# Kernel tuning notes

Measured on AMD Instinct MI355X. Metric: run time of the kernel, lower is better.

The kernel has to match this reference:

```python
import jax, jax.numpy as jnp
import numpy as np

NTYPE, NWAVE, NIPSIN = 4, 16, 3
CUTOFF = 5.0
NLOCAL, NALL, NNEIGH = 40000, 48000, 800000
# angular-order index for each of the npara = 1 + 3 + 9 = 13 angular channels
INDEX_PARA = np.concatenate([np.full(3 ** i, i, dtype=np.int32) for i in range(NIPSIN)])


def setup_inputs() -> dict:
    key = jax.random.key(0)
    k0, k1, k2, k3, k4, k5, k6 = jax.random.split(key, 7)
    cart = jax.random.normal(k0, (NALL, 3), dtype=jnp.float32) * 3.0
    i0 = jax.random.randint(k1, (NNEIGH,), 0, NLOCAL, dtype=jnp.int32)
    off = jax.random.randint(k2, (NNEIGH,), 1, NALL, dtype=jnp.int32)
    i1 = (i0 + off) % NALL  # guaranteed != i0 -> no zero distances
    atom_index = jnp.stack([i0, i1], axis=0)
    local_species = jax.random.randint(k3, (NLOCAL,), 0, NTYPE, dtype=jnp.int32)
    neigh_species = jax.random.randint(k4, (NNEIGH,), 0, NTYPE, dtype=jnp.int32)
    rs = jax.random.uniform(k5, (NTYPE, NWAVE), dtype=jnp.float32) * CUTOFF
    inta = 0.5 + jax.random.uniform(k6, (NTYPE, NWAVE), dtype=jnp.float32)
    params = jnp.ones((NTYPE, NWAVE), dtype=jnp.float32)
    return {"cart": cart, "rs": rs, "inta": inta, "params": params,
            "atom_index": atom_index, "local_species": local_species,
            "neigh_species": neigh_species}


def _density(cart, rs, inta, params, atom_index, nlocal, neigh_species):
    # gather neighbor pair coordinates: (2, n, 3)
    sel = cart[atom_index.reshape(-1)].reshape(2, -1, 3)
    dvec = sel[0] - sel[1]                               # (n, 3)
    dist = jnp.linalg.norm(dvec, axis=-1)                # (n,)
    dvec = dvec / dist[:, None]                          # unit vectors
    # cutoff_cosine
    fcut = jnp.square(0.5 * jnp.cos(dist * (np.pi / CUTOFF)) + 0.5)  # (n,)
    # species-gathered gaussian radial basis (vectorized form of per-type masked_scatter loop)
    radial = jnp.exp(-inta[neigh_species] * jnp.square(dist[:, None] - rs[neigh_species]))  # (n, nwave)
    # angular tensor-product channels: concat over orders 0..NIPSIN-1 -> (13, n)
    dvt = dvec.T                                         # (3, n)
    orb = fcut[None, :]                                  # (1, n)
    parts = [orb]
    for _ in range(1, NIPSIN):
        orb = (orb[:, None, :] * dvt[None, :, :]).reshape(-1, orb.shape[1])  # (3^p, n)
        parts.append(orb)
    angular = jnp.concatenate(parts, axis=0)             # (npara, n)
    # outer product per pair: (n, npara, nwave)
    orbital = jnp.einsum('ji,ik->ijk', angular, radial)
    worb = orbital * params[neigh_species][:, None, :]
    # scatter-add over central atoms
    sumw = jnp.zeros((nlocal, angular.shape[0], rs.shape[1]), worb.dtype)
    sumw = sumw.at[atom_index[0]].add(worb)              # (nlocal, npara, nwave)
    # reduce squared channels by angular order
    density = jnp.zeros((nlocal, NIPSIN, rs.shape[1]), worb.dtype)
    density = density.at[:, INDEX_PARA].add(jnp.square(sumw))
    return density.reshape(nlocal, -1)                   # (nlocal, nipsin*nwave)


def reference(cart, rs, inta, params, atom_index, local_species, neigh_species):
    nlocal = local_species.shape[0]
    return _density(cart, rs, inta, params, atom_index, nlocal, neigh_species)
```

## Files before the change

kernel.cpp:

```cpp
#include <hip/hip_runtime.h>
#include <hip/hip_bf16.h>

#define NWAVE 16
#define LOG2CHUNK 14
#define CHUNK (1 << LOG2CHUNK)
#define HIST_WORDS 10240

constexpr float PI_OVER_CUT = 3.14159265358979323846f / 5.0f;


__global__ __launch_bounds__(1024) void chunk_hist_rank(
    const int* __restrict__ idx0, unsigned short* __restrict__ lrank,
    unsigned short* __restrict__ hist16, int nneigh, int halfp)
{
    __shared__ unsigned lds[HIST_WORDS];
    int c = blockIdx.x >> 1;
    int parity = blockIdx.x & 1;
    int t = threadIdx.x;

    int words = halfp >> 1;
    for (int w = t; w < words; w += 1024) lds[w] = 0u;
    __syncthreads();

    int jbeg = c << LOG2CHUNK;
    int jend = jbeg + CHUNK; if (jend > nneigh) jend = nneigh;
    for (int j = jbeg + t; j < jend; j += 1024) {
        int a = idx0[j];
        if ((a & 1) == parity) {
            int bin = a >> 1;
            int word = bin >> 1;
            int shift = (bin & 1) << 4;
            unsigned old = atomicAdd(&lds[word], 1u << shift);
            lrank[j] = (unsigned short)((old >> shift) & 0xffffu);
        }
    }
    __syncthreads();

    unsigned* hrow = (unsigned*)(hist16 + (size_t)blockIdx.x * halfp);
    for (int w = t; w < words; w += 1024) hrow[w] = lds[w];
}


__global__ __launch_bounds__(256) void combine_pre(
    const unsigned short* __restrict__ hist16, unsigned* __restrict__ counts,
    unsigned short* __restrict__ chunkpre, int nlocal, int nc, int halfp)
{
    int a = blockIdx.x * blockDim.x + threadIdx.x;
    if (a >= nlocal) return;
    int parity = a & 1;
    int bin = a >> 1;
    unsigned run = 0;
    for (int c = 0; c < nc; ++c) {
        unsigned h = hist16[(size_t)(c*2 + parity) * halfp + bin];
        chunkpre[(size_t)a * nc + c] = (unsigned short)run;
        run += h;
    }
    counts[a] = run;
}


__global__ __launch_bounds__(256) void scan_partial(const unsigned* __restrict__ counts,
                                                    unsigned* __restrict__ partials, int n) {
    __shared__ unsigned wsum[4];
    int t = threadIdx.x;
    int base = blockIdx.x * 1024 + t * 4;
    unsigned s = 0;
    #pragma unroll
    for (int e = 0; e < 4; ++e) { int id = base + e; if (id < n) s += counts[id]; }
    #pragma unroll
    for (int off = 32; off >= 1; off >>= 1) s += __shfl_xor(s, off, 64);
    int lane = t & 63, w = t >> 6;
    if (lane == 0) wsum[w] = s;
    __syncthreads();
    if (t == 0) partials[blockIdx.x] = wsum[0] + wsum[1] + wsum[2] + wsum[3];
}

__global__ __launch_bounds__(64) void scan_blockoffs(const unsigned* __restrict__ partials,
                                                     unsigned* __restrict__ blockoff,
                                                     unsigned* __restrict__ offsets,
                                                     int nblk, int nlocal) {
    int t = threadIdx.x;
    unsigned v = (t < nblk) ? partials[t] : 0u;
    unsigned incl = v;
    #pragma unroll
    for (int off = 1; off < 64; off <<= 1) {
        unsigned u = __shfl_up(incl, off, 64);
        if (t >= off) incl += u;
    }
    if (t < nblk) blockoff[t] = incl - v;
    if (t == nblk - 1) offsets[nlocal] = incl;
}

__global__ __launch_bounds__(256) void scan_final(const unsigned* __restrict__ counts,
                                                  const unsigned* __restrict__ blockoff,
                                                  unsigned* __restrict__ offsets, int n) {
    __shared__ unsigned wsum[4];
    int t = threadIdx.x;
    int lane = t & 63, w = t >> 6;
    int base = blockIdx.x * 1024 + t * 4;
    unsigned c[4];
    #pragma unroll
    for (int e = 0; e < 4; ++e) { int id = base + e; c[e] = (id < n) ? counts[id] : 0u; }
    unsigned tsum = c[0] + c[1] + c[2] + c[3];
    unsigned incl = tsum;
    #pragma unroll
    for (int off = 1; off < 64; off <<= 1) {
        unsigned u = __shfl_up(incl, off, 64);
        if (lane >= off) incl += u;
    }
    if (lane == 63) wsum[w] = incl;
    __syncthreads();
    unsigned wpre = 0;
    for (int i = 0; i < 4; ++i) if (i < w) wpre += wsum[i];
    unsigned x = blockoff[blockIdx.x] + wpre + (incl - tsum);
    #pragma unroll
    for (int e = 0; e < 4; ++e) {
        int id = base + e;
        if (id < n) offsets[id] = x;
        x += c[e];
    }
}


__global__ __launch_bounds__(256) void geom_scatter_direct(
    const float* __restrict__ cart, const int* __restrict__ idx0,
    const int* __restrict__ idx1, const int* __restrict__ nspec,
    const unsigned short* __restrict__ lrank, const unsigned* __restrict__ offsets,
    const unsigned short* __restrict__ chunkpre, float4* __restrict__ srec,
    int nneigh, int nc)
{
    int j = blockIdx.x * blockDim.x + threadIdx.x;
    if (j >= nneigh) return;
    int i0 = idx0[j], i1 = idx1[j], s = nspec[j];
    int c = j >> LOG2CHUNK;
    unsigned p = offsets[i0] + (unsigned)chunkpre[(size_t)i0 * nc + c] + (unsigned)lrank[j];
    float ax = cart[3*i0], ay = cart[3*i0+1], az = cart[3*i0+2];
    float bx = cart[3*i1], by = cart[3*i1+1], bz = cart[3*i1+2];
    float dxv = ax - bx, dyv = ay - by, dzv = az - bz;
    float d2 = dxv*dxv + dyv*dyv + dzv*dzv;
    float rinv = rsqrtf(d2);
    float dist = d2 * rinv;
    unsigned db = (__float_as_uint(dist) & ~3u) | (unsigned)s;
    srec[p] = make_float4(dxv * rinv, dyv * rinv, dzv * rinv, __uint_as_float(db));
}


__global__ __launch_bounds__(256) void density_seq(
    const float* __restrict__ rs, const float* __restrict__ inta,
    const float* __restrict__ params, const unsigned* __restrict__ offsets,
    const float4* __restrict__ srec, float* __restrict__ out,
    int nlocal, int nneigh)
{
    int t = threadIdx.x;
    int lane = t & 63;
    int k = lane & 15, g = lane >> 4;
    int a = blockIdx.x * 4 + (t >> 6);
    if (a >= nlocal) return;

    float rs0 = rs[k],        rs1 = rs[16 + k],     rs2 = rs[32 + k],     rs3 = rs[48 + k];
    float ia0 = inta[k],      ia1 = inta[16 + k],   ia2 = inta[32 + k],   ia3 = inta[48 + k];
    float pp0 = params[k],    pp1 = params[16 + k], pp2 = params[32 + k], pp3 = params[48 + k];

    int beg = (int)offsets[a], end = (int)offsets[a + 1];
    int lim = nneigh - 1;

    float aw = 0.f, axl = 0.f, ayl = 0.f, azl = 0.f;
    float axx = 0.f, ayy = 0.f, azz = 0.f, axy = 0.f, axz = 0.f, ayz = 0.f;

    int p0 = beg + g; if (p0 > lim) p0 = lim;
    float4 rec0 = srec[p0];

    for (int n = beg; n < end; n += 4) {
        int p1 = n + 4 + g; if (p1 > lim) p1 = lim;
        float4 rec1 = srec[p1];

        unsigned u = __float_as_uint(rec0.w);
        float dist = __uint_as_float(u & ~3u);
        bool c1 = (u & 1u) != 0u, c2 = (u & 2u) != 0u;
        float rsel = c2 ? (c1 ? rs3 : rs2) : (c1 ? rs1 : rs0);
        float isel = c2 ? (c1 ? ia3 : ia2) : (c1 ? ia1 : ia0);
        float psel = c2 ? (c1 ? pp3 : pp2) : (c1 ? pp1 : pp0);
        float dd  = dist - rsel;
        float rad = __expf(-isel * dd * dd);
        float fc  = fmaf(0.5f, __cosf(dist * PI_OVER_CUT), 0.5f);
        float w   = rad * fc * fc * psel;
        w = (n + g < end) ? w : 0.f;

        float dx = rec0.x, dy = rec0.y, dz = rec0.z;
        float wx = w * dx, wy = w * dy, wz = w * dz;
        aw  += w;
        axl += wx;  ayl += wy;  azl += wz;
        axx = fmaf(wx, dx, axx);  axy = fmaf(wx, dy, axy);  axz = fmaf(wx, dz, axz);
        ayy = fmaf(wy, dy, ayy);  ayz = fmaf(wy, dz, ayz);  azz = fmaf(wz, dz, azz);

        rec0 = rec1;
    }

    #define RED2(x) x += __shfl_xor(x, 16, 64); x += __shfl_xor(x, 32, 64)
    RED2(aw); RED2(axl); RED2(ayl); RED2(azl);
    RED2(axx); RED2(ayy); RED2(azz); RED2(axy); RED2(axz); RED2(ayz);
    #undef RED2

    if (g == 0) {
        float l0 = aw * aw;
        float l1 = axl*axl + ayl*ayl + azl*azl;
        float l2 = axx*axx + ayy*ayy + azz*azz + 2.f*(axy*axy + axz*axz + ayz*ayz);
        out[a*48 + k]      = l0;
        out[a*48 + 16 + k] = l1;
        out[a*48 + 32 + k] = l2;
    }
}


__global__ void hist_kernel(const int* __restrict__ idx0, unsigned* __restrict__ counts, int nneigh) {
    int j = blockIdx.x * blockDim.x + threadIdx.x;
    if (j < nneigh) atomicAdd(&counts[idx0[j]], 1u);
}

__global__ void scan_kernel_1blk(const unsigned* __restrict__ counts, unsigned* __restrict__ offsets,
                                 unsigned* __restrict__ cursor, int nlocal) {
    __shared__ unsigned part[1024];
    int t = threadIdx.x;
    int ch = (nlocal + 1023) / 1024;
    int base = t * ch;
    unsigned s = 0;
    for (int i = 0; i < ch; ++i) { int id = base + i; if (id < nlocal) s += counts[id]; }
    part[t] = s;
    __syncthreads();
    for (int off = 1; off < 1024; off <<= 1) {
        unsigned v = (t >= off) ? part[t - off] : 0u;
        __syncthreads();
        part[t] += v;
        __syncthreads();
    }
    unsigned run = (t == 0) ? 0u : part[t - 1];
    for (int i = 0; i < ch; ++i) {
        int id = base + i;
        if (id < nlocal) { offsets[id] = run; cursor[id] = run; run += counts[id]; }
    }
    if (t == 1023) offsets[nlocal] = part[1023];
}

__global__ __launch_bounds__(256) void scatter_idx(const int* __restrict__ idx0,
                                                   unsigned* __restrict__ cursor,
                                                   unsigned* __restrict__ sorted, int nneigh) {
    int j = blockIdx.x * blockDim.x + threadIdx.x;
    if (j < nneigh) {
        unsigned p = atomicAdd(&cursor[idx0[j]], 1u);
        sorted[p] = (unsigned)j;
    }
}

__global__ __launch_bounds__(256) void density_kernel(
    const float* __restrict__ cart, const float* __restrict__ rs,
    const float* __restrict__ inta, const float* __restrict__ params,
    const int* __restrict__ idx1, const int* __restrict__ nspec,
    const unsigned* __restrict__ offsets, const unsigned* __restrict__ sorted,
    float* __restrict__ out, int nlocal)
{
    int lane = threadIdx.x & 63;
    int a = blockIdx.x * 4 + (threadIdx.x >> 6);
    if (a >= nlocal) return;
    int k = lane & 15;
    int g = lane >> 4;
    float c0x = cart[3*a], c0y = cart[3*a+1], c0z = cart[3*a+2];
    int a1, b1, a2, b2;
    switch (g) {
      case 0:  a1=0; b1=0; a2=1; b2=1; break;
      case 1:  a1=0; b1=1; a2=1; b2=2; break;
      case 2:  a1=0; b1=2; a2=2; b2=0; break;
      default: a1=1; b1=0; a2=2; b2=1; break;
    }
    float acc0 = 0.f, acc1 = 0.f, acc2 = 0.f, acc3 = 0.f;
    unsigned beg = offsets[a], end = offsets[a + 1];
    for (unsigned n = beg; n < end; ++n) {
        int j  = (int)sorted[n];
        int i1 = idx1[j];
        int s  = nspec[j];
        float dxv = c0x - cart[3*i1];
        float dyv = c0y - cart[3*i1+1];
        float dzv = c0z - cart[3*i1+2];
        float d2   = dxv*dxv + dyv*dyv + dzv*dzv;
        float rinv = rsqrtf(d2);
        float dist = d2 * rinv;
        float dx = dxv * rinv, dy = dyv * rinv, dz = dzv * rinv;
        float fc   = 0.5f * __cosf(dist * PI_OVER_CUT) + 0.5f;
        float fcut = fc * fc;
        float tt   = dist - rs[s*NWAVE + k];
        float rad  = __expf(-inta[s*NWAVE + k] * tt * tt) * params[s*NWAVE + k];
        float f1 = (g == 0) ? fcut : fcut * (g == 1 ? dx : (g == 2 ? dy : dz));
        acc0 = fmaf(f1, rad, acc0);
        float pa1 = (a1 == 0 ? dx : (a1 == 1 ? dy : dz));
        float pb1 = (b1 == 0 ? dx : (b1 == 1 ? dy : dz));
        acc1 = fmaf(fcut * pa1 * pb1, rad, acc1);
        float pa2 = (a2 == 0 ? dx : (a2 == 1 ? dy : dz));
        float pb2 = (b2 == 0 ? dx : (b2 == 1 ? dy : dz));
        acc2 = fmaf(fcut * pa2 * pb2, rad, acc2);
        if (g == 0) acc3 = fmaf(fcut * dz * dz, rad, acc3);
    }
    float l0, l1, l2;
    if (g == 0) { l0 = acc0*acc0; l1 = 0.f;        l2 = acc1*acc1 + acc2*acc2 + acc3*acc3; }
    else        { l0 = 0.f;       l1 = acc0*acc0;  l2 = acc1*acc1 + acc2*acc2; }
    l0 += __shfl_xor(l0, 16, 64); l1 += __shfl_xor(l1, 16, 64); l2 += __shfl_xor(l2, 16, 64);
    l0 += __shfl_xor(l0, 32, 64); l1 += __shfl_xor(l1, 32, 64); l2 += __shfl_xor(l2, 32, 64);
    if (g == 0) {
        out[a*48 + k]      = l0;
        out[a*48 + 16 + k] = l1;
        out[a*48 + 32 + k] = l2;
    }
}


extern "C" void kernel_launch(void* const* d_in, const int* in_sizes, int n_in,
                              void* d_out, int out_size, void* d_ws, size_t ws_size,
                              hipStream_t stream) {
    const float* cart   = (const float*)d_in[0];
    const float* rs     = (const float*)d_in[1];
    const float* inta   = (const float*)d_in[2];
    const float* params = (const float*)d_in[3];
    const int* atom_index    = (const int*)d_in[4];
    const int* neigh_species = (const int*)d_in[6];
    int nlocal = in_sizes[5];
    int nneigh = in_sizes[6];
    const int* idx0 = atom_index;
    const int* idx1 = atom_index + nneigh;

    int tb = 256;
    int nblkN = (nneigh + tb - 1) / tb;
    int nblkS = (nlocal + 1023) / 1024;
    int nc = (nneigh + CHUNK - 1) >> LOG2CHUNK;
    int halfp = (((nlocal + 1) >> 1) + 63) & ~63;

    char* ws = (char*)d_ws;
    size_t off = 0;
    auto carve = [&](size_t bytes) -> char* {
        off = (off + 255) & ~(size_t)255;
        char* p = ws + off; off += bytes; return p;
    };
    unsigned* counts        = (unsigned*)carve((size_t)nlocal * 4);
    unsigned* offsets       = (unsigned*)carve(((size_t)nlocal + 1) * 4);
    unsigned* cursor        = (unsigned*)carve((size_t)nlocal * 4);
    unsigned* partials      = (unsigned*)carve(256 * 4);
    unsigned* blockoff      = (unsigned*)carve(256 * 4);
    float4*   srec          = (float4*)carve((size_t)nneigh * 16);
    unsigned short* lrank   = (unsigned short*)carve((size_t)nneigh * 2);
    unsigned short* hist16  = (unsigned short*)carve((size_t)nc * 2 * halfp * 2);
    unsigned short* chunkpre= (unsigned short*)carve((size_t)nlocal * nc * 2);
    size_t need_fast = off;

    bool fast = (ws_size >= need_fast) && (nblkS <= 64) && (halfp <= 2 * HIST_WORDS) && (nc <= 64);

    if (fast) {
        chunk_hist_rank<<<nc * 2, 1024, 0, stream>>>(idx0, lrank, hist16, nneigh, halfp);
        combine_pre<<<(nlocal + tb - 1) / tb, tb, 0, stream>>>(hist16, counts, chunkpre,
                                                               nlocal, nc, halfp);
        scan_partial<<<nblkS, 256, 0, stream>>>(counts, partials, nlocal);
        scan_blockoffs<<<1, 64, 0, stream>>>(partials, blockoff, offsets, nblkS, nlocal);
        scan_final<<<nblkS, 256, 0, stream>>>(counts, blockoff, offsets, nlocal);
        geom_scatter_direct<<<nblkN, tb, 0, stream>>>(cart, idx0, idx1, neigh_species,
                                                      lrank, offsets, chunkpre, srec,
                                                      nneigh, nc);
        density_seq<<<(nlocal + 3) / 4, 256, 0, stream>>>(rs, inta, params, offsets, srec,
                                                          (float*)d_out, nlocal, nneigh);
    } else {
        unsigned* sorted = (unsigned*)srec;
        hipMemsetAsync(counts, 0, (size_t)nlocal * 4, stream);
        hist_kernel<<<nblkN, tb, 0, stream>>>(idx0, counts, nneigh);
        scan_kernel_1blk<<<1, 1024, 0, stream>>>(counts, offsets, cursor, nlocal);
        scatter_idx<<<nblkN, tb, 0, stream>>>(idx0, cursor, sorted, nneigh);
        density_kernel<<<(nlocal + 3) / 4, 256, 0, stream>>>(cart, rs, inta, params, idx1,
                                                             neigh_species, offsets, sorted,
                                                             (float*)d_out, nlocal);
    }
}
```

Before: 85.13 us.

## Fuse count/scan kernels and transpose chunk prefix table to chunk-major

Replaces the combine_pre plus three-kernel scan with two kernels: one computes per-block count partials straight from the chunk histograms, and the second scans block partials in-wave, computes per-atom offsets, and writes chunk prefixes. The chunk-prefix table becomes chunk-major so those writes coalesce, and reads in the scatter kernel fall within a single chunk row for neighbouring j. This cuts launch count and the intermediate counts/blockoff round trips, at the cost of reading the histograms twice.

```diff
diff --git a/kernel.cpp b/kernel.cpp
--- a/kernel.cpp
+++ b/kernel.cpp
@@ -41,83 +41,87 @@
 }
 
 
-__global__ __launch_bounds__(256) void combine_pre(
-    const unsigned short* __restrict__ hist16, unsigned* __restrict__ counts,
-    unsigned short* __restrict__ chunkpre, int nlocal, int nc, int halfp)
-{
-    int a = blockIdx.x * blockDim.x + threadIdx.x;
-    if (a >= nlocal) return;
-    int parity = a & 1;
-    int bin = a >> 1;
-    unsigned run = 0;
-    for (int c = 0; c < nc; ++c) {
-        unsigned h = hist16[(size_t)(c*2 + parity) * halfp + bin];
-        chunkpre[(size_t)a * nc + c] = (unsigned short)run;
-        run += h;
-    }
-    counts[a] = run;
-}
-
-
-__global__ __launch_bounds__(256) void scan_partial(const unsigned* __restrict__ counts,
-                                                    unsigned* __restrict__ partials, int n) {
-    __shared__ unsigned wsum[4];
-    int t = threadIdx.x;
-    int base = blockIdx.x * 1024 + t * 4;
-    unsigned s = 0;
+__global__ __launch_bounds__(1024) void count_partial(
+    const unsigned short* __restrict__ hist16, unsigned* __restrict__ partials,
+    int nlocal, int nc, int halfp)
+{
+    __shared__ unsigned wsum[16];
+    int t = threadIdx.x;
+    int lane = t & 63, wid = t >> 6;
+    int a = blockIdx.x * 1024 + t;
+    unsigned v = 0;
+    if (a < nlocal) {
+        int parity = a & 1, bin = a >> 1;
+        for (int c = 0; c < nc; ++c)
+            v += hist16[(size_t)(c * 2 + parity) * halfp + bin];
+    }
     #pragma unroll
-    for (int e = 0; e < 4; ++e) { int id = base + e; if (id < n) s += counts[id]; }
-    #pragma unroll
-    for (int off = 32; off >= 1; off >>= 1) s += __shfl_xor(s, off, 64);
-    int lane = t & 63, w = t >> 6;
-    if (lane == 0) wsum[w] = s;
-    __syncthreads();
-    if (t == 0) partials[blockIdx.x] = wsum[0] + wsum[1] + wsum[2] + wsum[3];
-}
-
-__global__ __launch_bounds__(64) void scan_blockoffs(const unsigned* __restrict__ partials,
-                                                     unsigned* __restrict__ blockoff,
-                                                     unsigned* __restrict__ offsets,
-                                                     int nblk, int nlocal) {
-    int t = threadIdx.x;
-    unsigned v = (t < nblk) ? partials[t] : 0u;
+    for (int o = 32; o >= 1; o >>= 1) v += __shfl_xor(v, o, 64);
+    if (lane == 0) wsum[wid] = v;
+    __syncthreads();
+    if (t == 0) {
+        unsigned s = 0;
+        #pragma unroll
+        for (int i = 0; i < 16; ++i) s += wsum[i];
+        partials[blockIdx.x] = s;
+    }
+}
+
+
+__global__ __launch_bounds__(1024) void scan_offsets_chunkpre(
+    const unsigned short* __restrict__ hist16, const unsigned* __restrict__ partials,
+    unsigned* __restrict__ offsets, unsigned short* __restrict__ chunkpreT,
+    int nlocal, int nblk, int nc, int halfp, int nlocalp)
+{
+    __shared__ unsigned wsum[16];
+    __shared__ unsigned sOff;
+    int t = threadIdx.x;
+    int lane = t & 63, wid = t >> 6;
+    int a = blockIdx.x * 1024 + t;
+
+    if (wid == 0) {
+        unsigned p = (lane < nblk) ? partials[lane] : 0u;
+        unsigned incl = p;
+        #pragma unroll
+        for (int o = 1; o < 64; o <<= 1) {
+            unsigned u = __shfl_up(incl, o, 64);
+            if (lane >= o) incl += u;
+        }
+        if (lane == blockIdx.x) sOff = incl - p;
+    }
+
+    unsigned v = 0;
+    if (a < nlocal) {
+        int parity = a & 1, bin = a >> 1;
+        for (int c = 0; c < nc; ++c) {
+            chunkpreT[(size_t)c * nlocalp + a] = (unsigned short)v;
+            v += hist16[(size_t)(c * 2 + parity) * halfp + bin];
+        }
+    }
+
     unsigned incl = v;
     #pragma unroll
-    for (int off = 1; off < 64; off <<= 1) {
-        unsigned u = __shfl_up(incl, off, 64);
-        if (t >= off) incl += u;
-    }
-    if (t < nblk) blockoff[t] = incl - v;
-    if (t == nblk - 1) offsets[nlocal] = incl;
-}
-
-__global__ __launch_bounds__(256) void scan_final(const unsigned* __restrict__ counts,
-                                                  const unsigned* __restrict__ blockoff,
-                                                  unsigned* __restrict__ offsets, int n) {
-    __shared__ unsigned wsum[4];
-    int t = threadIdx.x;
-    int lane = t & 63, w = t >> 6;
-    int base = blockIdx.x * 1024 + t * 4;
-    unsigned c[4];
-    #pragma unroll
-    for (int e = 0; e < 4; ++e) { int id = base + e; c[e] = (id < n) ? counts[id] : 0u; }
-    unsigned tsum = c[0] + c[1] + c[2] + c[3];
-    unsigned incl = tsum;
-    #pragma unroll
-    for (int off = 1; off < 64; off <<= 1) {
-        unsigned u = __shfl_up(incl, off, 64);
-        if (lane >= off) incl += u;
-    }
-    if (lane == 63) wsum[w] = incl;
-    __syncthreads();
-    unsigned wpre = 0;
-    for (int i = 0; i < 4; ++i) if (i < w) wpre += wsum[i];
-    unsigned x = blockoff[blockIdx.x] + wpre + (incl - tsum);
-    #pragma unroll
-    for (int e = 0; e < 4; ++e) {
-        int id = base + e;
-        if (id < n) offsets[id] = x;
-        x += c[e];
+    for (int o = 1; o < 64; o <<= 1) {
+        unsigned u = __shfl_up(incl, o, 64);
+        if (lane >= o) incl += u;
+    }
+    if (lane == 63) wsum[wid] = incl;
+    __syncthreads();
+    if (t < 16) {
+        unsigned u = wsum[t];
+        unsigned wincl = u;
+        #pragma unroll
+        for (int o = 1; o < 16; o <<= 1) {
+            unsigned x = __shfl_up(wincl, o, 64);
+            if (t >= o) wincl += x;
+        }
+        wsum[t] = wincl - u;
+    }
+    __syncthreads();
+    if (a < nlocal) {
+        unsigned o = sOff + wsum[wid] + (incl - v);
+        offsets[a] = o;
+        if (a == nlocal - 1) offsets[nlocal] = o + v;
     }
 }
 
@@ -126,14 +130,15 @@
     const float* __restrict__ cart, const int* __restrict__ idx0,
     const int* __restrict__ idx1, const int* __restrict__ nspec,
     const unsigned short* __restrict__ lrank, const unsigned* __restrict__ offsets,
-    const unsigned short* __restrict__ chunkpre, float4* __restrict__ srec,
-    int nneigh, int nc)
+    const unsigned short* __restrict__ chunkpreT, float4* __restrict__ srec,
+    int nneigh, int nlocalp)
 {
     int j = blockIdx.x * blockDim.x + threadIdx.x;
     if (j >= nneigh) return;
     int i0 = idx0[j], i1 = idx1[j], s = nspec[j];
     int c = j >> LOG2CHUNK;
-    unsigned p = offsets[i0] + (unsigned)chunkpre[(size_t)i0 * nc + c] + (unsigned)lrank[j];
+    unsigned p = offsets[i0] + (unsigned)chunkpreT[(size_t)c * nlocalp + i0]
+                             + (unsigned)lrank[j];
     float ax = cart[3*i0], ay = cart[3*i0+1], az = cart[3*i0+2];
     float bx = cart[3*i1], by = cart[3*i1+1], bz = cart[3*i1+2];
     float dxv = ax - bx, dyv = ay - by, dzv = az - bz;
@@ -327,9 +332,10 @@
 
     int tb = 256;
     int nblkN = (nneigh + tb - 1) / tb;
-    int nblkS = (nlocal + 1023) / 1024;
     int nc = (nneigh + CHUNK - 1) >> LOG2CHUNK;
     int halfp = (((nlocal + 1) >> 1) + 63) & ~63;
+    int nlocalp = (nlocal + 63) & ~63;
+    int nblkB = (nlocal + 1023) / 1024;
 
     char* ws = (char*)d_ws;
     size_t off = 0;
@@ -341,25 +347,24 @@
     unsigned* offsets       = (unsigned*)carve(((size_t)nlocal + 1) * 4);
     unsigned* cursor        = (unsigned*)carve((size_t)nlocal * 4);
     unsigned* partials      = (unsigned*)carve(256 * 4);
-    unsigned* blockoff      = (unsigned*)carve(256 * 4);
     float4*   srec          = (float4*)carve((size_t)nneigh * 16);
     unsigned short* lrank   = (unsigned short*)carve((size_t)nneigh * 2);
     unsigned short* hist16  = (unsigned short*)carve((size_t)nc * 2 * halfp * 2);
-    unsigned short* chunkpre= (unsigned short*)carve((size_t)nlocal * nc * 2);
+    unsigned short* chunkpreT = (unsigned short*)carve((size_t)nc * nlocalp * 2);
     size_t need_fast = off;
 
-    bool fast = (ws_size >= need_fast) && (nblkS <= 64) && (halfp <= 2 * HIST_WORDS) && (nc <= 64);
+    bool fast = (ws_size >= need_fast) && (nblkB <= 64) &&
+                (halfp <= 2 * HIST_WORDS) && (nc <= 64);
 
     if (fast) {
         chunk_hist_rank<<<nc * 2, 1024, 0, stream>>>(idx0, lrank, hist16, nneigh, halfp);
-        combine_pre<<<(nlocal + tb - 1) / tb, tb, 0, stream>>>(hist16, counts, chunkpre,
-                                                               nlocal, nc, halfp);
-        scan_partial<<<nblkS, 256, 0, stream>>>(counts, partials, nlocal);
-        scan_blockoffs<<<1, 64, 0, stream>>>(partials, blockoff, offsets, nblkS, nlocal);
-        scan_final<<<nblkS, 256, 0, stream>>>(counts, blockoff, offsets, nlocal);
+        count_partial<<<nblkB, 1024, 0, stream>>>(hist16, partials, nlocal, nc, halfp);
+        scan_offsets_chunkpre<<<nblkB, 1024, 0, stream>>>(hist16, partials, offsets,
+                                                          chunkpreT, nlocal, nblkB, nc,
+                                                          halfp, nlocalp);
         geom_scatter_direct<<<nblkN, tb, 0, stream>>>(cart, idx0, idx1, neigh_species,
-                                                      lrank, offsets, chunkpre, srec,
-                                                      nneigh, nc);
+                                                      lrank, offsets, chunkpreT, srec,
+                                                      nneigh, nlocalp);
         density_seq<<<(nlocal + 3) / 4, 256, 0, stream>>>(rs, inta, params, offsets, srec,
                                                           (float*)d_out, nlocal, nneigh);
     } else {
```

After: 80.17 us. -5.8%, faster.
